# Optimization experiments

Hardware: AMD Instinct MI355X
Metric: run time of the kernel (lower is better)

Reference implementation:

```python
import jax, jax.numpy as jnp
import numpy as np

B, S, H = 16, 2048, 1024

def setup_inputs() -> dict:
    key = jax.random.key(0)
    ks = jax.random.split(key, 6)
    return {
        "h": jax.random.normal(ks[0], (1, B, H), jnp.float32),
        "c": jax.random.normal(ks[1], (1, B, H), jnp.float32),
        "encoder_outputs": jax.random.normal(ks[2], (B, S, H), jnp.float32),
        "attn_W": jax.random.normal(ks[3], (H, 2 * H), jnp.float32) * 0.02,
        "attn_b": jax.random.normal(ks[4], (H,), jnp.float32) * 0.02,
        "v_W": jax.random.normal(ks[5], (1, H), jnp.float32) * 0.02,
    }

def reference(h, c, encoder_outputs, attn_W, attn_b, v_W):
    # h: (1,B,H) -> (B,1,H); a: (B,S,H)
    a = encoder_outputs
    hq = jnp.transpose(h, (1, 0, 2))  # (B,1,H)
    # cat((s, a), -1) @ attn_W.T == s @ Wh.T + a @ Wa.T (avoids (B,S,2H) buffer)
    Wh, Wa = attn_W[:, :H], attn_W[:, H:]
    energy = jax.nn.relu(
        jnp.einsum("bqh,oh->bqo", hq, Wh)          # (B,1,H), broadcast over S
        + jnp.einsum("bsh,oh->bso", a, Wa)
        + attn_b
    )  # (B,S,H)
    scores = jnp.einsum("bsh,h->bs", energy, v_W[0])  # (B,S)
    attn_weights = jax.nn.softmax(scores, axis=1)      # (B,S)
    context = jnp.einsum("bs,bsh->bh", attn_weights, a)[:, None, :]  # (B,1,H)
    return context, attn_weights
```

## Files before the change

### kernel.cpp

```cpp
#include <hip/hip_runtime.h>
#include <hip/hip_bf16.h>


typedef __bf16 bf16x8 __attribute__((ext_vector_type(8)));
typedef float floatx4 __attribute__((ext_vector_type(4)));

#define BB 16
#define SS 2048
#define HH 1024
#define MM (BB * SS)

#define GLB(p) ((const __attribute__((address_space(1))) void*)(p))
#define LDSP(p) ((__attribute__((address_space(3))) void*)(p))

__device__ inline ushort f2bf(float x) {
    uint32_t u = __builtin_bit_cast(uint32_t, x);
    u += 0x7FFFu + ((u >> 16) & 1u);
    return (ushort)(u >> 16);
}

__global__ __launch_bounds__(256) void convert_A_kernel(
    const float* __restrict__ src, __bf16* __restrict__ dst)
{
    size_t i = (size_t)blockIdx.x * 256 + threadIdx.x;
    const float* s = src + i * 8;
    float4 a = *(const float4*)(s);
    float4 b = *(const float4*)(s + 4);
    union { ushort u[8]; uint4 v; } p;
    p.u[0] = f2bf(a.x); p.u[1] = f2bf(a.y); p.u[2] = f2bf(a.z); p.u[3] = f2bf(a.w);
    p.u[4] = f2bf(b.x); p.u[5] = f2bf(b.y); p.u[6] = f2bf(b.z); p.u[7] = f2bf(b.w);
    *(uint4*)(dst + i * 8) = p.v;
}

__global__ __launch_bounds__(256) void prep_kernel(
    const float* __restrict__ h, const float* __restrict__ W,
    const float* __restrict__ bias, float* __restrict__ projh,
    __bf16* __restrict__ Wb, float* __restrict__ scores, float* __restrict__ ctx)
{
    int bid = blockIdx.x;
    int tid = threadIdx.x;
    if (bid < 256) {
        int b = bid >> 4;
        int oc = bid & 15;
        __shared__ float hrow[HH];
        *(float4*)&hrow[tid * 4] = *(const float4*)(h + (size_t)b * HH + tid * 4);
        __syncthreads();
        int ol = tid >> 2;
        int kq = tid & 3;
        int o = oc * 64 + ol;
        const float* wr = W + (size_t)o * (2 * HH) + kq * 256;
        const float* hb = hrow + kq * 256;
        float sum = 0.f;
        for (int k = 0; k < 256; k += 4) {
            float4 wv = *(const float4*)(wr + k);
            sum += hb[k] * wv.x + hb[k + 1] * wv.y + hb[k + 2] * wv.z + hb[k + 3] * wv.w;
        }
        sum += __shfl_xor(sum, 1);
        sum += __shfl_xor(sum, 2);
        if (kq == 0) projh[b * HH + o] = sum + bias[o];
    } else if (bid < 320) {
        int cb = bid - 256;
#pragma unroll
        for (int j = 0; j < 8; j++) {
            int g = cb * 2048 + tid + j * 256;
            int o = g >> 7;
            int k = (g & 127) * 8;
            const float* s = W + (size_t)o * (2 * HH) + HH + k;
            float4 a = *(const float4*)(s);
            float4 b2 = *(const float4*)(s + 4);
            union { ushort u[8]; uint4 v; } p;
            p.u[0] = f2bf(a.x); p.u[1] = f2bf(a.y); p.u[2] = f2bf(a.z); p.u[3] = f2bf(a.w);
            p.u[4] = f2bf(b2.x); p.u[5] = f2bf(b2.y); p.u[6] = f2bf(b2.z); p.u[7] = f2bf(b2.w);
            *(uint4*)(Wb + (size_t)o * HH + k) = p.v;
        }
    } else {
        int zb = bid - 320;
        float4 z = make_float4(0.f, 0.f, 0.f, 0.f);
        float* sp = scores + zb * 2048 + tid * 8;
        *(float4*)(sp) = z;
        *(float4*)(sp + 4) = z;
        *(float4*)(ctx + zb * 1024 + tid * 4) = z;
    }
}

__global__ __launch_bounds__(512, 2) void gemm_scores_kernel(
    const __bf16* __restrict__ Ab,
    const __bf16* __restrict__ Wb,
    const float* __restrict__ projh,
    const float* __restrict__ vW,
    float* __restrict__ scores)
{
    __shared__ __bf16 smem[32768];

    const int bid = blockIdx.x;
    const int m0 = (((bid >> 5) << 3) + (bid & 7)) * 256;
    const int n0 = ((bid >> 3) & 3) * 256;
    const int bidx = m0 >> 11;

    const int tid = threadIdx.x;
    const int lane = tid & 63;
    const int wave = tid >> 6;
    const int wm = (wave & 1) * 128;
    const int wn = (wave >> 1) * 64;
    const int quad = lane >> 4;
    const int l16 = lane & 15;

    floatx4 acc[8][4];
    const floatx4 z = {0.f, 0.f, 0.f, 0.f};
#pragma unroll
    for (int i = 0; i < 8; i++)
#pragma unroll
        for (int j = 0; j < 4; j++) acc[i][j] = z;

    {
    }
    const int su = tid >> 3;
    const int sj = (tid & 7) ^ (su & 7);
    const int g_row = su * 2 + (sj >> 2);
    const int g_col = (sj & 3) * 8;
    const __bf16* gA  = Ab + (size_t)(m0 + g_row) * HH + g_col;
    const __bf16* gA2 = gA + (size_t)128 * HH;
    const __bf16* gB  = Wb + (size_t)(n0 + g_row) * HH + g_col;
    const __bf16* gB2 = gB + (size_t)128 * HH;
    const int ldsb = wave * 512;

    int aoff[8], boff[4];
#pragma unroll
    for (int i = 0; i < 8; i++) {
        int frow = wm + i * 16 + l16;
        int u2 = frow >> 1;
        int cc = u2 * 8 + (((((frow & 1) << 2) | quad)) ^ (u2 & 7));
        aoff[i] = cc * 8;
    }
#pragma unroll
    for (int j = 0; j < 4; j++) {
        int frow = wn + j * 16 + l16;
        int u2 = frow >> 1;
        int cc = u2 * 8 + (((((frow & 1) << 2) | quad)) ^ (u2 & 7));
        boff[j] = 8192 + cc * 8;
    }

#define ISSUE_STAGE(buf, k0)                                                          \
    {                                                                                 \
        __bf16* dst = smem + (buf) * 16384 + ldsb;                                    \
        __builtin_amdgcn_global_load_lds(GLB(gA  + (k0)), LDSP(dst),         16, 0, 0); \
        __builtin_amdgcn_global_load_lds(GLB(gA2 + (k0)), LDSP(dst + 4096),  16, 0, 0); \
        __builtin_amdgcn_global_load_lds(GLB(gB  + (k0)), LDSP(dst + 8192),  16, 0, 0); \
        __builtin_amdgcn_global_load_lds(GLB(gB2 + (k0)), LDSP(dst + 12288), 16, 0, 0); \
    }

    ISSUE_STAGE(0, 0)
    for (int s = 0; s < 32; s++) {
        __syncthreads();
        if (s < 31) ISSUE_STAGE((s + 1) & 1, (s + 1) * 32)
        const __bf16* sb = smem + (s & 1) * 16384;
        bf16x8 af[8], bfr[4];
#pragma unroll
        for (int j = 0; j < 4; j++) bfr[j] = *(const bf16x8*)(sb + boff[j]);
#pragma unroll
        for (int i = 0; i < 8; i++) af[i] = *(const bf16x8*)(sb + aoff[i]);
#pragma unroll
        for (int i = 0; i < 8; i++)
#pragma unroll
            for (int j = 0; j < 4; j++)
                acc[i][j] = __builtin_amdgcn_mfma_f32_16x16x32_bf16(af[i], bfr[j], acc[i][j], 0, 0, 0);
    }
#undef ISSUE_STAGE

    float ph[4], vv[4];
#pragma unroll
    for (int j = 0; j < 4; j++) {
        int ng = n0 + wn + j * 16 + l16;
        ph[j] = projh[bidx * HH + ng];
        vv[j] = vW[ng];
    }
#pragma unroll
    for (int i = 0; i < 8; i++) {
        float s[4] = {0.f, 0.f, 0.f, 0.f};
#pragma unroll
        for (int j = 0; j < 4; j++) {
#pragma unroll
            for (int r2 = 0; r2 < 4; r2++) {
                float e = acc[i][j][r2] + ph[j];
                e = e > 0.f ? e : 0.f;
                s[r2] += e * vv[j];
            }
        }
#pragma unroll
        for (int r2 = 0; r2 < 4; r2++) {
            s[r2] += __shfl_xor(s[r2], 1);
            s[r2] += __shfl_xor(s[r2], 2);
            s[r2] += __shfl_xor(s[r2], 4);
            s[r2] += __shfl_xor(s[r2], 8);
        }
        if (l16 == 0) {
#pragma unroll
            for (int r2 = 0; r2 < 4; r2++) {
                int mg = m0 + wm + i * 16 + quad * 4 + r2;
                atomicAdd(&scores[mg], s[r2]);
            }
        }
    }
}

__global__ __launch_bounds__(256) void gemm_scores_f32_kernel(
    const float* __restrict__ A, const float* __restrict__ W,
    const float* __restrict__ projh, const float* __restrict__ vW,
    float* __restrict__ scores)
{
    constexpr int BM = 128, BN = 128, BK = 32, LDT = BK + 8;
    __shared__ __bf16 As[BM * LDT];
    __shared__ __bf16 Bs[BN * LDT];
    const int n0 = blockIdx.x * BN;
    const int m0 = blockIdx.y * BM;
    const int bidx = m0 >> 11;
    const int tid = threadIdx.x;
    const int lane = tid & 63;
    const int wave = tid >> 6;
    const int wm = (wave & 1) * 64;
    const int wn = (wave >> 1) * 64;
    const int quad = lane >> 4;
    const int l16 = lane & 15;
    floatx4 acc[4][4];
    const floatx4 z = {0.f, 0.f, 0.f, 0.f};
#pragma unroll
    for (int i = 0; i < 4; i++)
#pragma unroll
        for (int j = 0; j < 4; j++) acc[i][j] = z;
    int rowT[4], colT[4];
#pragma unroll
    for (int i = 0; i < 4; i++) {
        int fi = tid + 256 * i;
        rowT[i] = fi >> 3;
        colT[i] = (fi & 7) * 4;
    }
    for (int k0 = 0; k0 < HH; k0 += BK) {
        float4 av[4], bv[4];
#pragma unroll
        for (int i = 0; i < 4; i++) {
            av[i] = *(const float4*)(A + (size_t)(m0 + rowT[i]) * HH + k0 + colT[i]);
            bv[i] = *(const float4*)(W + (size_t)(n0 + rowT[i]) * (2 * HH) + HH + k0 + colT[i]);
        }
        __syncthreads();
#pragma unroll
        for (int i = 0; i < 4; i++) {
            ushort4 ua = make_ushort4(f2bf(av[i].x), f2bf(av[i].y), f2bf(av[i].z), f2bf(av[i].w));
            ushort4 ub = make_ushort4(f2bf(bv[i].x), f2bf(bv[i].y), f2bf(bv[i].z), f2bf(bv[i].w));
            *(ushort4*)&As[rowT[i] * LDT + colT[i]] = ua;
            *(ushort4*)&Bs[rowT[i] * LDT + colT[i]] = ub;
        }
        __syncthreads();
        bf16x8 af[4], bf[4];
#pragma unroll
        for (int i = 0; i < 4; i++)
            af[i] = *(const bf16x8*)&As[(wm + i * 16 + l16) * LDT + quad * 8];
#pragma unroll
        for (int j = 0; j < 4; j++)
            bf[j] = *(const bf16x8*)&Bs[(wn + j * 16 + l16) * LDT + quad * 8];
#pragma unroll
        for (int i = 0; i < 4; i++)
#pragma unroll
            for (int j = 0; j < 4; j++)
                acc[i][j] = __builtin_amdgcn_mfma_f32_16x16x32_bf16(af[i], bf[j], acc[i][j], 0, 0, 0);
    }
    float ph[4], vv[4];
#pragma unroll
    for (int j = 0; j < 4; j++) {
        int ng = n0 + wn + j * 16 + l16;
        ph[j] = projh[bidx * HH + ng];
        vv[j] = vW[ng];
    }
#pragma unroll
    for (int i = 0; i < 4; i++) {
        float s[4] = {0.f, 0.f, 0.f, 0.f};
#pragma unroll
        for (int j = 0; j < 4; j++) {
#pragma unroll
            for (int r = 0; r < 4; r++) {
                float e = acc[i][j][r] + ph[j];
                e = e > 0.f ? e : 0.f;
                s[r] += e * vv[j];
            }
        }
#pragma unroll
        for (int r = 0; r < 4; r++) {
            s[r] += __shfl_xor(s[r], 1);
            s[r] += __shfl_xor(s[r], 2);
            s[r] += __shfl_xor(s[r], 4);
            s[r] += __shfl_xor(s[r], 8);
        }
        if (l16 == 0) {
#pragma unroll
            for (int r = 0; r < 4; r++) {
                int mg = m0 + wm + i * 16 + quad * 4 + r;
                atomicAdd(&scores[mg], s[r]);
            }
        }
    }
}

__global__ __launch_bounds__(256) void softmax_kernel(
    const float* __restrict__ scores, float* __restrict__ wout)
{
    int b = blockIdx.x;
    int tid = threadIdx.x;
    const float* row = scores + b * SS;
    float x[8];
    float mx = -1e30f;
#pragma unroll
    for (int i = 0; i < 8; i++) { x[i] = row[tid + i * 256]; mx = fmaxf(mx, x[i]); }
#pragma unroll
    for (int off = 32; off; off >>= 1) mx = fmaxf(mx, __shfl_xor(mx, off));
    __shared__ float redm[4], reds[4];
    if ((tid & 63) == 0) redm[tid >> 6] = mx;
    __syncthreads();
    mx = fmaxf(fmaxf(redm[0], redm[1]), fmaxf(redm[2], redm[3]));
    float sum = 0.f;
#pragma unroll
    for (int i = 0; i < 8; i++) { x[i] = __expf(x[i] - mx); sum += x[i]; }
#pragma unroll
    for (int off = 32; off; off >>= 1) sum += __shfl_xor(sum, off);
    if ((tid & 63) == 0) reds[tid >> 6] = sum;
    __syncthreads();
    float inv = 1.0f / (reds[0] + reds[1] + reds[2] + reds[3]);
#pragma unroll
    for (int i = 0; i < 8; i++) wout[b * SS + tid + i * 256] = x[i] * inv;
}

__global__ __launch_bounds__(256) void context_kernel(
    const float* __restrict__ A, const float* __restrict__ wgt, float* __restrict__ ctx)
{
    int b = blockIdx.x >> 5;
    int sc = blockIdx.x & 31;
    int tid = threadIdx.x;
    const float* arow = A + ((size_t)b * SS + sc * 64) * HH + tid * 4;
    const float* wrow = wgt + b * SS + sc * 64;
    float4 acc = make_float4(0.f, 0.f, 0.f, 0.f);
#pragma unroll 4
    for (int s = 0; s < 64; s++) {
        float w = wrow[s];
        float4 v = *(const float4*)(arow + (size_t)s * HH);
        acc.x += w * v.x; acc.y += w * v.y; acc.z += w * v.z; acc.w += w * v.w;
    }
    float* o = ctx + b * HH + tid * 4;
    atomicAdd(o + 0, acc.x);
    atomicAdd(o + 1, acc.y);
    atomicAdd(o + 2, acc.z);
    atomicAdd(o + 3, acc.w);
}

extern "C" void kernel_launch(void* const* d_in, const int* in_sizes, int n_in,
                              void* d_out, int out_size, void* d_ws, size_t ws_size,
                              hipStream_t stream) {
    const float* h    = (const float*)d_in[0];
    const float* a    = (const float*)d_in[2];
    const float* W    = (const float*)d_in[3];
    const float* bias = (const float*)d_in[4];
    const float* vW   = (const float*)d_in[5];
    float* out = (float*)d_out;

    float* projh  = (float*)d_ws;
    float* scores = projh + BB * HH;
    __bf16* Wb = (__bf16*)(scores + MM);
    __bf16* Ab = Wb + (size_t)HH * HH;
    const size_t need = (size_t)(BB * HH + MM) * 4 + (size_t)HH * HH * 2
                      + (size_t)MM * HH * 2;

    if (ws_size >= need) {
        prep_kernel<<<336, 256, 0, stream>>>(h, W, bias, projh, Wb, scores, out);
        convert_A_kernel<<<(MM * HH / 8) / 256, 256, 0, stream>>>(a, Ab);
        gemm_scores_kernel<<<512, 512, 0, stream>>>(Ab, Wb, projh, vW, scores);
    } else {
        prep_kernel<<<336, 256, 0, stream>>>(h, W, bias, projh, Wb, scores, out);
        gemm_scores_f32_kernel<<<dim3(HH / 128, MM / 128), 256, 0, stream>>>(a, W, projh, vW, scores);
    }

    softmax_kernel<<<BB, 256, 0, stream>>>(scores, out + BB * HH);
    context_kernel<<<BB * 32, 256, 0, stream>>>(a, out + BB * HH, out);
}
```

Measured before the change: 309.1 us.

## Fuse prep with A conversion and softmax with context to cut launches

```diff
diff --git a/kernel.cpp b/kernel.cpp
--- a/kernel.cpp
+++ b/kernel.cpp
@@ -19,27 +19,24 @@
     return (ushort)(u >> 16);
 }
 
-__global__ __launch_bounds__(256) void convert_A_kernel(
-    const float* __restrict__ src, __bf16* __restrict__ dst)
-{
-    size_t i = (size_t)blockIdx.x * 256 + threadIdx.x;
-    const float* s = src + i * 8;
-    float4 a = *(const float4*)(s);
-    float4 b = *(const float4*)(s + 4);
-    union { ushort u[8]; uint4 v; } p;
-    p.u[0] = f2bf(a.x); p.u[1] = f2bf(a.y); p.u[2] = f2bf(a.z); p.u[3] = f2bf(a.w);
-    p.u[4] = f2bf(b.x); p.u[5] = f2bf(b.y); p.u[6] = f2bf(b.z); p.u[7] = f2bf(b.w);
-    *(uint4*)(dst + i * 8) = p.v;
-}
-
-__global__ __launch_bounds__(256) void prep_kernel(
+__global__ __launch_bounds__(256) void prep_all_kernel(
     const float* __restrict__ h, const float* __restrict__ W,
-    const float* __restrict__ bias, float* __restrict__ projh,
-    __bf16* __restrict__ Wb, float* __restrict__ scores, float* __restrict__ ctx)
+    const float* __restrict__ bias, const float* __restrict__ a,
+    float* __restrict__ projh, __bf16* __restrict__ Wb, __bf16* __restrict__ Ab,
+    float* __restrict__ scores, float* __restrict__ ctx)
 {
     int bid = blockIdx.x;
     int tid = threadIdx.x;
-    if (bid < 256) {
+    if (bid >= 336) {
+        size_t i = (size_t)(bid - 336) * 256 + tid;
+        const float* s = a + i * 8;
+        float4 x = *(const float4*)(s);
+        float4 y = *(const float4*)(s + 4);
+        union { ushort u[8]; uint4 v; } p;
+        p.u[0] = f2bf(x.x); p.u[1] = f2bf(x.y); p.u[2] = f2bf(x.z); p.u[3] = f2bf(x.w);
+        p.u[4] = f2bf(y.x); p.u[5] = f2bf(y.y); p.u[6] = f2bf(y.z); p.u[7] = f2bf(y.w);
+        *(uint4*)(Ab + i * 8) = p.v;
+    } else if (bid < 256) {
         int b = bid >> 4;
         int oc = bid & 15;
         __shared__ float hrow[HH];
@@ -66,11 +63,11 @@
             int o = g >> 7;
             int k = (g & 127) * 8;
             const float* s = W + (size_t)o * (2 * HH) + HH + k;
-            float4 a = *(const float4*)(s);
-            float4 b2 = *(const float4*)(s + 4);
+            float4 x = *(const float4*)(s);
+            float4 y = *(const float4*)(s + 4);
             union { ushort u[8]; uint4 v; } p;
-            p.u[0] = f2bf(a.x); p.u[1] = f2bf(a.y); p.u[2] = f2bf(a.z); p.u[3] = f2bf(a.w);
-            p.u[4] = f2bf(b2.x); p.u[5] = f2bf(b2.y); p.u[6] = f2bf(b2.z); p.u[7] = f2bf(b2.w);
+            p.u[0] = f2bf(x.x); p.u[1] = f2bf(x.y); p.u[2] = f2bf(x.z); p.u[3] = f2bf(x.w);
+            p.u[4] = f2bf(y.x); p.u[5] = f2bf(y.y); p.u[6] = f2bf(y.z); p.u[7] = f2bf(y.w);
             *(uint4*)(Wb + (size_t)o * HH + k) = p.v;
         }
     } else {
@@ -112,8 +109,6 @@
 #pragma unroll
         for (int j = 0; j < 4; j++) acc[i][j] = z;
 
-    {
-    }
     const int su = tid >> 3;
     const int sj = (tid & 7) ^ (su & 7);
     const int g_row = su * 2 + (sj >> 2);
@@ -299,16 +294,19 @@
     }
 }
 
-__global__ __launch_bounds__(256) void softmax_kernel(
-    const float* __restrict__ scores, float* __restrict__ wout)
+__global__ __launch_bounds__(256) void softmax_context_kernel(
+    const float* __restrict__ A, const float* __restrict__ scores,
+    float* __restrict__ wout, float* __restrict__ ctx)
 {
-    int b = blockIdx.x;
+    int b = blockIdx.x >> 5;
+    int sc = blockIdx.x & 31;
     int tid = threadIdx.x;
-    const float* row = scores + b * SS;
+    const float* srow = scores + b * SS;
+
     float x[8];
     float mx = -1e30f;
 #pragma unroll
-    for (int i = 0; i < 8; i++) { x[i] = row[tid + i * 256]; mx = fmaxf(mx, x[i]); }
+    for (int i = 0; i < 8; i++) { x[i] = srow[tid + i * 256]; mx = fmaxf(mx, x[i]); }
 #pragma unroll
     for (int off = 32; off; off >>= 1) mx = fmaxf(mx, __shfl_xor(mx, off));
     __shared__ float redm[4], reds[4];
@@ -317,28 +315,26 @@
     mx = fmaxf(fmaxf(redm[0], redm[1]), fmaxf(redm[2], redm[3]));
     float sum = 0.f;
 #pragma unroll
-    for (int i = 0; i < 8; i++) { x[i] = __expf(x[i] - mx); sum += x[i]; }
+    for (int i = 0; i < 8; i++) sum += __expf(x[i] - mx);
 #pragma unroll
     for (int off = 32; off; off >>= 1) sum += __shfl_xor(sum, off);
     if ((tid & 63) == 0) reds[tid >> 6] = sum;
     __syncthreads();
     float inv = 1.0f / (reds[0] + reds[1] + reds[2] + reds[3]);
-#pragma unroll
-    for (int i = 0; i < 8; i++) wout[b * SS + tid + i * 256] = x[i] * inv;
-}
-
-__global__ __launch_bounds__(256) void context_kernel(
-    const float* __restrict__ A, const float* __restrict__ wgt, float* __restrict__ ctx)
-{
-    int b = blockIdx.x >> 5;
-    int sc = blockIdx.x & 31;
-    int tid = threadIdx.x;
+
+    __shared__ float wsm[64];
+    if (tid < 64) {
+        float wv = __expf(srow[sc * 64 + tid] - mx) * inv;
+        wsm[tid] = wv;
+        wout[b * SS + sc * 64 + tid] = wv;
+    }
+    __syncthreads();
+
     const float* arow = A + ((size_t)b * SS + sc * 64) * HH + tid * 4;
-    const float* wrow = wgt + b * SS + sc * 64;
     float4 acc = make_float4(0.f, 0.f, 0.f, 0.f);
 #pragma unroll 4
     for (int s = 0; s < 64; s++) {
-        float w = wrow[s];
+        float w = wsm[s];
         float4 v = *(const float4*)(arow + (size_t)s * HH);
         acc.x += w * v.x; acc.y += w * v.y; acc.z += w * v.z; acc.w += w * v.w;
     }
@@ -367,14 +363,13 @@
                       + (size_t)MM * HH * 2;
 
     if (ws_size >= need) {
-        prep_kernel<<<336, 256, 0, stream>>>(h, W, bias, projh, Wb, scores, out);
-        convert_A_kernel<<<(MM * HH / 8) / 256, 256, 0, stream>>>(a, Ab);
+        prep_all_kernel<<<336 + MM * HH / 8 / 256, 256, 0, stream>>>(
+            h, W, bias, a, projh, Wb, Ab, scores, out);
         gemm_scores_kernel<<<512, 512, 0, stream>>>(Ab, Wb, projh, vW, scores);
     } else {
-        prep_kernel<<<336, 256, 0, stream>>>(h, W, bias, projh, Wb, scores, out);
+        prep_all_kernel<<<336, 256, 0, stream>>>(h, W, bias, a, projh, Wb, Ab, scores, out);
         gemm_scores_f32_kernel<<<dim3(HH / 128, MM / 128), 256, 0, stream>>>(a, W, projh, vW, scores);
     }
 
-    softmax_kernel<<<BB, 256, 0, stream>>>(scores, out + BB * HH);
-    context_kernel<<<BB * 32, 256, 0, stream>>>(a, out + BB * HH, out);
-}
+    softmax_context_kernel<<<BB * 32, 256, 0, stream>>>(a, scores, out + BB * HH, out);
+}
```

New measurement: 295.0 us. -4.6%, faster.
